# Optimization experiments

Hardware: AMD Instinct MI355X
Metric: run time of the kernel (lower is better)

The kernel has to match this reference:

```python
import jax, jax.numpy as jnp
import numpy as np

B, L_TOT, C = 64, 8192, 4
WIN = 16
H = 64
NL = 8
GROUPS = 8          # head groups
SA_GROUP = 4        # SortAttn group (hard-coded default)
GH = H * 2 // SA_GROUP   # 32
SEG = 4
CLS = 4
IN_SIZE = C * WIN   # 64 == H (all layers share input dim)


def _shuffle(x):
    # torch Shuffle: transpose(-1,-2).contiguous().view(original_shape)
    return jnp.swapaxes(x, -1, -2).reshape(x.shape)


def setup_inputs() -> dict:
    key = jax.random.key(0)
    ks = jax.random.split(key, 32)
    s = 0.1
    f32 = jnp.float32
    return {
        "x": jax.random.normal(ks[0], (B, L_TOT, C), f32),
        "h0_param": jnp.zeros((NL, 1, H), f32),
        "gru_w_ih": (jax.random.normal(ks[1], (NL, 3 * H, IN_SIZE), f32) * s),
        "gru_w_hh": (jax.random.normal(ks[2], (NL, 3 * H, H), f32) * s),
        "gru_b_ih": (jax.random.normal(ks[3], (NL, 3 * H), f32) * s),
        "gru_b_hh": (jax.random.normal(ks[4], (NL, 3 * H), f32) * s),
        "attn_w1": (jax.random.normal(ks[5], (NL, H, H), f32) * s),
        "attn_w2": (jax.random.normal(ks[6], (NL, GH, GH), f32) * s),
        "attn_w3": (jax.random.normal(ks[7], (NL, GH, GH), f32) * s),
        "attn_w4": (jax.random.normal(ks[8], (NL, H, 2 * H), f32) * s),
        "seg_w1": (jax.random.normal(ks[9], (SEG, H // GROUPS), f32) * s),
        "seg_b1": (jax.random.normal(ks[10], (SEG,), f32) * s),
        "seg_w2": (jax.random.normal(ks[11], (SEG, SEG), f32) * s),
        "seg_b2": (jax.random.normal(ks[12], (SEG,), f32) * s),
        "seg_w3": (jax.random.normal(ks[13], (SEG, SEG), f32) * s),
        "seg_b3": (jax.random.normal(ks[14], (SEG,), f32) * s),
        "seg_w4": (jax.random.normal(ks[15], (WIN, GROUPS), f32) * s),
        "seg_b4": (jax.random.normal(ks[16], (WIN,), f32) * s),
        "cls_w1": (jax.random.normal(ks[17], (CLS, H // GROUPS), f32) * s),
        "cls_b1": (jax.random.normal(ks[18], (CLS,), f32) * s),
        "cls_w2": (jax.random.normal(ks[19], (CLS, CLS), f32) * s),
        "cls_b2": (jax.random.normal(ks[20], (CLS,), f32) * s),
        "cls_w3": (jax.random.normal(ks[21], (CLS, CLS), f32) * s),
        "cls_b3": (jax.random.normal(ks[22], (CLS,), f32) * s),
        "cls_w4": (jax.random.normal(ks[23], (CLS, CLS * GROUPS), f32) * s),
        "cls_b4": (jax.random.normal(ks[24], (CLS,), f32) * s),
    }


def reference(x, h0_param, gru_w_ih, gru_w_hh, gru_b_ih, gru_b_hh,
              attn_w1, attn_w2, attn_w3, attn_w4,
              seg_w1, seg_b1, seg_w2, seg_b2, seg_w3, seg_b3, seg_w4, seg_b4,
              cls_w1, cls_b1, cls_w2, cls_b2, cls_w3, cls_b3, cls_w4, cls_b4):
    b, l, c = x.shape
    lw = l // WIN
    xs = x.reshape(b, lw, WIN * c)                     # (b, lw, IN_SIZE)
    h0 = jnp.broadcast_to(h0_param, (NL, b, H))        # hidden_0 * ones(1,b,1)

    def gru_cell(inp, h, w_ih, w_hh, b_ih, b_hh):
        gi = inp @ w_ih.T + b_ih                       # (b, 3H)
        gh = h @ w_hh.T + b_hh
        i_r, i_z, i_n = jnp.split(gi, 3, axis=1)
        h_r, h_z, h_n = jnp.split(gh, 3, axis=1)
        r = jax.nn.sigmoid(i_r + h_r)
        z = jax.nn.sigmoid(i_z + h_z)
        n = jnp.tanh(i_n + r * h_n)
        return (1.0 - z) * n + z * h

    def sort_attn(h, w1, w2, w3, w4):
        se = jnp.stack([h, jnp.sort(h, axis=1)], axis=1)   # (b, 2, H)
        a = se @ w1.T                                       # (b, 2, H)
        a = a.reshape(b, SA_GROUP, GH)                      # Flatten+Unflatten
        a = _shuffle(a) @ w2.T
        a = jax.nn.relu(_shuffle(a) @ w3.T)
        scores = jax.nn.sigmoid(a.reshape(b, SA_GROUP * GH) @ w4.T)  # (b, H)
        return h * scores

    def step(hidden, xt):
        inp = xt
        new = []
        for i in range(NL):
            hi = gru_cell(inp, hidden[i], gru_w_ih[i], gru_w_hh[i], gru_b_ih[i], gru_b_hh[i])
            hi = sort_attn(hi, attn_w1[i], attn_w2[i], attn_w3[i], attn_w4[i])
            new.append(hi)
            inp = hi
        return jnp.stack(new, axis=0), inp

    h_final, outs = jax.lax.scan(step, h0, jnp.swapaxes(xs, 0, 1))
    ys = jnp.swapaxes(outs, 0, 1)                      # (b, lw, H)

    # ---- seg head ----
    t = ys.reshape(b, lw, GROUPS, H // GROUPS)         # (b, lw, 8, 8)
    t = t @ seg_w1.T + seg_b1                          # (b, lw, 8, 4)
    t = _shuffle(t) @ seg_w2.T + seg_b2
    t = _shuffle(t) @ seg_w3.T + seg_b3
    t = t.reshape(b, lw, SEG, GROUPS)                  # Flatten(2)+Unflatten
    t = t @ seg_w4.T + seg_b4
    seg = jnp.swapaxes(t, -1, -2).reshape(b, lw * WIN, SEG)  # (b, l, 4)

    # ---- avg_pool1d(k=11, s=1) with 10 zero history frames ----
    pool_in = jnp.concatenate([jnp.zeros((b, 10, SEG), seg.dtype), seg], axis=1)
    cs = jnp.concatenate([jnp.zeros((b, 1, SEG), seg.dtype),
                          jnp.cumsum(pool_in, axis=1)], axis=1)
    pool_seg = (cs[:, 11:] - cs[:, :-11]) / 11.0       # (b, l, 4)

    # ---- cls head ----
    u = ys.reshape(b * lw, GROUPS, H // GROUPS)
    u = u @ cls_w1.T + cls_b1
    u = _shuffle(u) @ cls_w2.T + cls_b2
    u = jax.nn.relu(_shuffle(u) @ cls_w3.T + cls_b3)
    cls = u.reshape(b * lw, CLS * GROUPS) @ cls_w4.T + cls_b4
    cls = cls.reshape(b, lw, CLS).mean(axis=1)         # (b, 4)

    return (pool_seg, cls, ys, h_final, seg)
```

## Files before the change

kernel.cpp:

```cpp
#include <hip/hip_runtime.h>
#include <math.h>

#define LW  512

typedef unsigned short u16;
typedef float f32x4 __attribute__((ext_vector_type(4)));
typedef u16 u16x4 __attribute__((ext_vector_type(4)));
typedef u16 u16x8 __attribute__((ext_vector_type(8)));
typedef unsigned u32x2v __attribute__((ext_vector_type(2)));
typedef __bf16 bf16x8 __attribute__((ext_vector_type(8)));

__device__ __forceinline__ u16 f2bf(float f) {
    return __builtin_bit_cast(u16, (__bf16)f);
}
__device__ __forceinline__ float bf2f(u16 h) {
    unsigned u = ((unsigned)h) << 16;
    return __builtin_bit_cast(float, u);
}
__device__ __forceinline__ float sigm(float x) {
    return __builtin_amdgcn_rcpf(1.0f + __expf(-x));
}
__device__ __forceinline__ float tanhfast(float x) {
    return 1.0f - 2.0f * __builtin_amdgcn_rcpf(1.0f + __expf(2.0f * x));
}
__device__ __forceinline__ f32x4 mfma16(u16x8 a, u16x8 b, f32x4 c) {
    return __builtin_amdgcn_mfma_f32_16x16x32_bf16(
        __builtin_bit_cast(bf16x8, a), __builtin_bit_cast(bf16x8, b), c, 0, 0, 0);
}
__device__ __forceinline__ u16x8 ld8_8al(const u16* p) {
    u16x4 lo = *(const u16x4*)p;
    u16x4 hi = *(const u16x4*)(p + 4);
    return __builtin_shufflevector(lo, hi, 0, 1, 2, 3, 4, 5, 6, 7);
}
__device__ __forceinline__ unsigned ld_sys(const unsigned* p) {
    return __hip_atomic_load(p, __ATOMIC_RELAXED, __HIP_MEMORY_SCOPE_SYSTEM);
}
__device__ __forceinline__ void st_sys(unsigned* p, unsigned v) {
    __hip_atomic_store(p, v, __ATOMIC_RELAXED, __HIP_MEMORY_SCOPE_SYSTEM);
}
__device__ __forceinline__ void poll_ge(const unsigned* p, unsigned want) {
    while (ld_sys(p) < want) __builtin_amdgcn_s_sleep(2);
    asm volatile("" ::: "memory");
    __builtin_amdgcn_sched_barrier(0);
}
__device__ __forceinline__ void poll4(const unsigned* p, unsigned want) {
    for (;;) {
        unsigned m0 = ld_sys(p + 0), m1 = ld_sys(p + 1);
        unsigned m2 = ld_sys(p + 2), m3 = ld_sys(p + 3);
        unsigned a = m0 < m1 ? m0 : m1;
        unsigned b = m2 < m3 ? m2 : m3;
        if ((a < b ? a : b) >= want) break;
        __builtin_amdgcn_s_sleep(2);
    }
    asm volatile("" ::: "memory");
    __builtin_amdgcn_sched_barrier(0);
}
__device__ __forceinline__ void bar_lgkm() {
    asm volatile("s_waitcnt lgkmcnt(0)" ::: "memory");
    __builtin_amdgcn_s_barrier();
}

template<int CTRL> __device__ __forceinline__ float dppf(float v) {
    return __builtin_bit_cast(float,
        __builtin_amdgcn_mov_dpp(__builtin_bit_cast(int, v), CTRL, 0xF, 0xF, false));
}
template<int OFF> __device__ __forceinline__ float swzf(float v) {
    return __builtin_bit_cast(float,
        __builtin_amdgcn_ds_swizzle(__builtin_bit_cast(int, v), OFF));
}
template<int J> __device__ __forceinline__ float xch(float v) {
    if constexpr (J == 1)  return dppf<0xB1>(v);
    else if constexpr (J == 2)  return dppf<0x4E>(v);
    else if constexpr (J == 4)  return swzf<0x101F>(v);
    else if constexpr (J == 8)  return swzf<0x201F>(v);
    else if constexpr (J == 16) return swzf<0x401F>(v);
    else return __shfl_xor(v, 32);
}
#define STG(KK, J) { \
    float o0 = xch<J>(v0), o1 = xch<J>(v1); \
    bool keepmin = (((ln & KK) == 0) == ((ln & J) == 0)); \
    v0 = keepmin ? fminf(v0, o0) : fmaxf(v0, o0); \
    v1 = keepmin ? fminf(v1, o1) : fmaxf(v1, o1); }

__global__ __launch_bounds__(256) void init_flags(unsigned* f) {
    f[blockIdx.x * 256 + threadIdx.x] = 0u;
}

__global__ __launch_bounds__(256, 1) void rnn_kernel(
    const float* __restrict__ x, const float* __restrict__ h0,
    const float* __restrict__ w_ih, const float* __restrict__ w_hh,
    const float* __restrict__ bih, const float* __restrict__ bhh,
    const float* __restrict__ aw1, const float* __restrict__ aw2,
    const float* __restrict__ aw3, const float* __restrict__ aw4,
    float* __restrict__ ys, float* __restrict__ hfin,
    unsigned* __restrict__ flags, unsigned* __restrict__ ring32, int D)
{
    const int l   = blockIdx.x >> 3;
    const int g   = blockIdx.x & 7;
    const int bb0 = g * 8;
    const int tid = threadIdx.x;
    const int w   = tid >> 6;
    const int ln  = tid & 63;
    const int l15 = ln & 15;
    const int l4  = ln >> 4;
    const bool bp = (D < LW);

    unsigned* myflag = flags + (size_t)(l * 8 + g) * 32;
    unsigned* pflag  = flags + (size_t)((l - 1) * 8 + g) * 32;
    unsigned* myccnt = flags + 4096 + (size_t)(l * 8 + g) * 32;
    unsigned* nccnt  = flags + 4096 + (size_t)((l + 1) * 8 + g) * 32;

    __shared__ __align__(16) u16 Hin[2][16][72];
    __shared__ __align__(16) u16 hbf[16][72];
    __shared__ __align__(16) u16 se [16][72];
    __shared__ __align__(16) u16 a23[32][36];
    __shared__ __align__(16) u16 w4A[16][136];

    for (int i = tid; i < 16 * 72; i += 256) {
        int r = i / 72, c = i % 72;
        if (r >= 8) { Hin[0][r][c] = 0; Hin[1][r][c] = 0; hbf[r][c] = 0; }
    }
    for (int i = tid; i < 16 * 136; i += 256) {
        int r = i / 136;
        if (r >= 8) w4A[r][i % 136] = 0;
    }

    const int o = 16 * w + l15;
    auto ldw8 = [](const float* p) {
        float4 v0 = *(const float4*)p;
        float4 v1 = *(const float4*)(p + 4);
        u16x8 r;
        r[0] = f2bf(v0.x); r[1] = f2bf(v0.y); r[2] = f2bf(v0.z); r[3] = f2bf(v0.w);
        r[4] = f2bf(v1.x); r[5] = f2bf(v1.y); r[6] = f2bf(v1.z); r[7] = f2bf(v1.w);
        return r;
    };
    const float* ih = w_ih + l * 12288;
    const float* hh = w_hh + l * 12288;
    u16x8 Br[4], Bz[4], Bni[2], Bnh[2], B1f[2], B2f[2], B3f[2], B4f[4];
    Br[0] = ldw8(ih + o * 64 + l4 * 8);        Br[1] = ldw8(ih + o * 64 + 32 + l4 * 8);
    Br[2] = ldw8(hh + o * 64 + l4 * 8);        Br[3] = ldw8(hh + o * 64 + 32 + l4 * 8);
    Bz[0] = ldw8(ih + (64 + o) * 64 + l4 * 8); Bz[1] = ldw8(ih + (64 + o) * 64 + 32 + l4 * 8);
    Bz[2] = ldw8(hh + (64 + o) * 64 + l4 * 8); Bz[3] = ldw8(hh + (64 + o) * 64 + 32 + l4 * 8);
    Bni[0] = ldw8(ih + (128 + o) * 64 + l4 * 8); Bni[1] = ldw8(ih + (128 + o) * 64 + 32 + l4 * 8);
    Bnh[0] = ldw8(hh + (128 + o) * 64 + l4 * 8); Bnh[1] = ldw8(hh + (128 + o) * 64 + 32 + l4 * 8);
    B1f[0] = ldw8(aw1 + l * 4096 + o * 64 + l4 * 8);
    B1f[1] = ldw8(aw1 + l * 4096 + o * 64 + 32 + l4 * 8);
    B2f[0] = ldw8(aw2 + l * 1024 + l15 * 32 + l4 * 8);
    B2f[1] = ldw8(aw2 + l * 1024 + (16 + l15) * 32 + l4 * 8);
    B3f[0] = ldw8(aw3 + l * 1024 + l15 * 32 + l4 * 8);
    B3f[1] = ldw8(aw3 + l * 1024 + (16 + l15) * 32 + l4 * 8);
    #pragma unroll
    for (int kk = 0; kk < 4; ++kk)
        B4f[kk] = ldw8(aw4 + l * 8192 + o * 128 + kk * 32 + l4 * 8);

    const float brs  = bih[l * 192 + o]       + bhh[l * 192 + o];
    const float bzs  = bih[l * 192 + 64 + o]  + bhh[l * 192 + 64 + o];
    const float bnis = bih[l * 192 + 128 + o];
    const float bnhs = bhh[l * 192 + 128 + o];

    float hreg[4];
    {
        float hv = h0[l * 64 + o];
        #pragma unroll
        for (int j = 0; j < 4; ++j) hreg[j] = hv;
        if (l4 < 2) {
            u16 hb = f2bf(hv);
            #pragma unroll
            for (int j = 0; j < 4; ++j) hbf[l4 * 4 + j][o] = hb;
        }
    }

    float4 stf = {0.f, 0.f, 0.f, 0.f};
    unsigned st0 = 0, st1 = 0;
    if (w >= 2) {
        const int rr = (tid - 128) >> 4, c4 = ((tid - 128) & 15) * 4;
        if (l == 0) {
            float4 a = *(const float4*)(x + (size_t)(bb0 + rr) * 32768 + c4);
            u16x4 hv;
            hv[0] = f2bf(a.x); hv[1] = f2bf(a.y); hv[2] = f2bf(a.z); hv[3] = f2bf(a.w);
            *(u16x4*)&Hin[0][rr][c4] = hv;
            stf = *(const float4*)(x + (size_t)(bb0 + rr) * 32768 + 64 + c4);
        } else {
            poll4(pflag, 1u);
            const unsigned* sp0 = ring32 + ((size_t)((l - 1) * 8 + g) * D + 0) * 256 + rr * 32 + (c4 >> 1);
            unsigned a0 = ld_sys(sp0), a1 = ld_sys(sp0 + 1);
            u32x2v dv = {a0, a1};
            *(u16x4*)&Hin[0][rr][c4] = __builtin_bit_cast(u16x4, dv);
            poll4(pflag, 2u);
            const unsigned* sp1 = ring32 + ((size_t)((l - 1) * 8 + g) * D + 1) * 256 + rr * 32 + (c4 >> 1);
            st0 = ld_sys(sp1); st1 = ld_sys(sp1 + 1);
        }
    }
    __syncthreads();

    u16x8 pAg0 = *(const u16x8*)&Hin[0][l15][l4 * 8];
    u16x8 pAg1 = *(const u16x8*)&Hin[0][l15][32 + l4 * 8];

    for (int t = 0; t < LW; ++t) {
        float hg[4];
        {
            u16x8 Ah0 = *(const u16x8*)&hbf[l15][l4 * 8];
            u16x8 Ah1 = *(const u16x8*)&hbf[l15][32 + l4 * 8];
            f32x4 z4 = {0.f, 0.f, 0.f, 0.f};
            f32x4 aR = z4, aZ = z4, aNI = z4, aNH = z4;
            aR = mfma16(pAg0, Br[0], aR);  aR = mfma16(pAg1, Br[1], aR);
            aR = mfma16(Ah0, Br[2], aR);   aR = mfma16(Ah1, Br[3], aR);
            aZ = mfma16(pAg0, Bz[0], aZ);  aZ = mfma16(pAg1, Bz[1], aZ);
            aZ = mfma16(Ah0, Bz[2], aZ);   aZ = mfma16(Ah1, Bz[3], aZ);
            aNI = mfma16(pAg0, Bni[0], aNI); aNI = mfma16(pAg1, Bni[1], aNI);
            aNH = mfma16(Ah0, Bnh[0], aNH);  aNH = mfma16(Ah1, Bnh[1], aNH);
            #pragma unroll
            for (int j = 0; j < 4; ++j) {
                float r  = sigm(aR[j] + brs);
                float zz = sigm(aZ[j] + bzs);
                float nn = tanhfast(aNI[j] + bnis + r * (aNH[j] + bnhs));
                hg[j] = (1.0f - zz) * nn + zz * hreg[j];
            }
            if (l4 < 2) {
                #pragma unroll
                for (int j = 0; j < 4; ++j) se[l4 * 4 + j][o] = f2bf(hg[j]);
            }
        }
        bar_lgkm();

        {
            float v0 = bf2f(se[2 * w][ln]);
            float v1 = bf2f(se[2 * w + 1][ln]);
            STG(2, 1)
            STG(4, 2)  STG(4, 1)
            STG(8, 4)  STG(8, 2)  STG(8, 1)
            STG(16, 8) STG(16, 4) STG(16, 2) STG(16, 1)
            STG(32, 16) STG(32, 8) STG(32, 4) STG(32, 2) STG(32, 1)
            STG(64, 32) STG(64, 16) STG(64, 8) STG(64, 4) STG(64, 2) STG(64, 1)
            se[8 + 2 * w][ln] = f2bf(v0);
            se[9 + 2 * w][ln] = f2bf(v1);
        }
        bar_lgkm();

        if (l < 7) {
            asm volatile("s_waitcnt vmcnt(0)" ::: "memory");
            if (ln == 0) st_sys(myflag + w, (unsigned)t);
        }
        {
            u16x8 As0 = *(const u16x8*)&se[l15][l4 * 8];
            u16x8 As1 = *(const u16x8*)&se[l15][32 + l4 * 8];
            f32x4 c = {0.f, 0.f, 0.f, 0.f};
            c = mfma16(As0, B1f[0], c);
            c = mfma16(As1, B1f[1], c);
            #pragma unroll
            for (int j = 0; j < 4; ++j) {
                int m = l4 * 4 + j;
                int p = m >> 3, b = m & 7;
                int f = p * 64 + o;
                int q = (f & 31) * 4 + (f >> 5);
                a23[b * 4 + (q >> 5)][q & 31] = f2bf(c[j]);
            }
        }
        bar_lgkm();

        if (w < 2) {
            const int Rb0 = 16 * w;
            u16x8 a2a = ld8_8al(&a23[Rb0 + l15][l4 * 8]);
            f32x4 z4 = {0.f, 0.f, 0.f, 0.f};
            f32x4 c2[2];
            c2[0] = mfma16(a2a, B2f[0], z4);
            c2[1] = mfma16(a2a, B2f[1], z4);
            #pragma unroll
            for (int nt = 0; nt < 2; ++nt)
                #pragma unroll
                for (int j = 0; j < 4; ++j) {
                    int m = Rb0 + l4 * 4 + j;
                    int b = m >> 2, i2 = m & 3;
                    int n = 16 * nt + l15;
                    int f2 = i2 * 32 + n;
                    int q2 = (f2 & 31) * 4 + (f2 >> 5);
                    a23[b * 4 + (q2 >> 5)][q2 & 31] = f2bf(c2[nt][j]);
                }
            asm volatile("s_waitcnt lgkmcnt(0)" ::: "memory");
            __builtin_amdgcn_sched_barrier(0);
            u16x8 a3a = ld8_8al(&a23[Rb0 + l15][l4 * 8]);
            f32x4 c3[2];
            c3[0] = mfma16(a3a, B3f[0], z4);
            c3[1] = mfma16(a3a, B3f[1], z4);
            #pragma unroll
            for (int nt = 0; nt < 2; ++nt)
                #pragma unroll
                for (int j = 0; j < 4; ++j) {
                    int m = Rb0 + l4 * 4 + j;
                    int b = m >> 2, i3 = m & 3;
                    int n = 16 * nt + l15;
                    w4A[b][i3 * 32 + n] = f2bf(fmaxf(c3[nt][j], 0.0f));
                }
        } else {
            const int rr = (tid - 128) >> 4, c4 = ((tid - 128) & 15) * 4;
            if (t + 1 < LW) {
                u16x4 hv;
                if (l == 0) {
                    hv[0] = f2bf(stf.x); hv[1] = f2bf(stf.y);
                    hv[2] = f2bf(stf.z); hv[3] = f2bf(stf.w);
                } else {
                    u32x2v dv = {st0, st1};
                    hv = __builtin_bit_cast(u16x4, dv);
                }
                *(u16x4*)&Hin[(t + 1) & 1][rr][c4] = hv;
            }
            if (t + 2 < LW) {
                if (l == 0) {
                    stf = *(const float4*)(x + (size_t)(bb0 + rr) * 32768 + (t + 2) * 64 + c4);
                } else {
                    poll4(pflag, (unsigned)(t + 3));
                    const unsigned* sp = ring32
                        + ((size_t)((l - 1) * 8 + g) * D + ((t + 2) & (D - 1))) * 256
                        + rr * 32 + (c4 >> 1);
                    st0 = ld_sys(sp); st1 = ld_sys(sp + 1);
                }
            }
        }
        bar_lgkm();
        if (bp && l > 0 && tid == 0)
            st_sys(myccnt, (unsigned)(t + 2));

        {
            u16x8 A40 = *(const u16x8*)&w4A[l15][l4 * 8];
            u16x8 A41 = *(const u16x8*)&w4A[l15][32 + l4 * 8];
            u16x8 A42 = *(const u16x8*)&w4A[l15][64 + l4 * 8];
            u16x8 A43 = *(const u16x8*)&w4A[l15][96 + l4 * 8];
            pAg0 = *(const u16x8*)&Hin[(t + 1) & 1][l15][l4 * 8];
            pAg1 = *(const u16x8*)&Hin[(t + 1) & 1][l15][32 + l4 * 8];
            f32x4 cs = {0.f, 0.f, 0.f, 0.f};
            cs = mfma16(A40, B4f[0], cs);
            cs = mfma16(A41, B4f[1], cs);
            cs = mfma16(A42, B4f[2], cs);
            cs = mfma16(A43, B4f[3], cs);

            if (bp && l < 7 && t >= D) {
                poll_ge(nccnt, (unsigned)(t - D + 1));
            }
            unsigned* slotp = ring32 + ((size_t)(l * 8 + g) * D + (t & (D - 1))) * 256;
            float hn[4]; u16 hb[4];
            #pragma unroll
            for (int j = 0; j < 4; ++j) {
                hn[j] = hg[j] * sigm(cs[j]);
                hreg[j] = hn[j];
                hb[j] = f2bf(hn[j]);
            }
            if (l4 < 2) {
                #pragma unroll
                for (int j = 0; j < 4; ++j) {
                    int row = l4 * 4 + j;
                    hbf[row][o] = hb[j];
                    if (l == 7) ys[(((size_t)(bb0 + row) << 9) + t) * 64 + o] = hn[j];
                    if (t == 511) hfin[((l << 6) + bb0 + row) * 64 + o] = hn[j];
                }
            }
            if (l < 7) {
                #pragma unroll
                for (int j = 0; j < 4; ++j) {
                    unsigned ob = (unsigned)__shfl_xor((int)(unsigned)hb[j], 1) & 0xffffu;
                    if (l4 < 2 && !(l15 & 1)) {
                        unsigned word = (unsigned)hb[j] | (ob << 16);
                        st_sys(&slotp[(l4 * 4 + j) * 32 + (o >> 1)], word);
                    }
                }
            }
        }
        bar_lgkm();
    }

    if (l < 7) {
        asm volatile("s_waitcnt vmcnt(0)" ::: "memory");
        if (ln == 0) st_sys(myflag + w, 512u);
    }
}

__global__ __launch_bounds__(256) void heads_kernel(
    const float* __restrict__ ys,
    const float* __restrict__ sw1, const float* __restrict__ sb1,
    const float* __restrict__ sw2, const float* __restrict__ sb2,
    const float* __restrict__ sw3, const float* __restrict__ sb3,
    const float* __restrict__ sw4, const float* __restrict__ sb4,
    const float* __restrict__ cw1, const float* __restrict__ cb1,
    const float* __restrict__ cw2, const float* __restrict__ cb2,
    const float* __restrict__ cw3, const float* __restrict__ cb3,
    const float* __restrict__ cw4, const float* __restrict__ cb4,
    float* __restrict__ seg_out, float* __restrict__ cls_tmp)
{
    const int idx = blockIdx.x * 256 + threadIdx.x;
    if (idx >= 64 * LW) return;
    const int b = idx >> 9, t = idx & 511;

    float y[64];
    const float4* yp = (const float4*)(ys + (size_t)idx * 64);
    #pragma unroll
    for (int i = 0; i < 16; ++i) {
        float4 v = yp[i];
        y[4 * i + 0] = v.x; y[4 * i + 1] = v.y; y[4 * i + 2] = v.z; y[4 * i + 3] = v.w;
    }

    float t1[8][4], t2[8][4], t3[8][4];

    #pragma unroll
    for (int g = 0; g < 8; ++g)
        #pragma unroll
        for (int s = 0; s < 4; ++s) {
            float acc = sb1[s];
            #pragma unroll
            for (int k = 0; k < 8; ++k) acc = fmaf(y[g * 8 + k], sw1[s * 8 + k], acc);
            t1[g][s] = acc;
        }
    #pragma unroll
    for (int i = 0; i < 8; ++i) {
        float sh[4];
        #pragma unroll
        for (int j = 0; j < 4; ++j) { int m = i * 4 + j; sh[j] = t1[m & 7][m >> 3]; }
        #pragma unroll
        for (int s = 0; s < 4; ++s) {
            float acc = sb2[s];
            #pragma unroll
            for (int j = 0; j < 4; ++j) acc = fmaf(sh[j], sw2[s * 4 + j], acc);
            t2[i][s] = acc;
        }
    }
    #pragma unroll
    for (int i = 0; i < 8; ++i) {
        float sh[4];
        #pragma unroll
        for (int j = 0; j < 4; ++j) { int m = i * 4 + j; sh[j] = t2[m & 7][m >> 3]; }
        #pragma unroll
        for (int s = 0; s < 4; ++s) {
            float acc = sb3[s];
            #pragma unroll
            for (int j = 0; j < 4; ++j) acc = fmaf(sh[j], sw3[s * 4 + j], acc);
            t3[i][s] = acc;
        }
    }
    #pragma unroll
    for (int w = 0; w < 16; ++w) {
        float o4[4];
        #pragma unroll
        for (int s = 0; s < 4; ++s) {
            float acc = sb4[w];
            #pragma unroll
            for (int j = 0; j < 8; ++j) {
                int f = s * 8 + j;
                acc = fmaf(t3[f >> 2][f & 3], sw4[w * 8 + j], acc);
            }
            o4[s] = acc;
        }
        float4 vv = {o4[0], o4[1], o4[2], o4[3]};
        ((float4*)seg_out)[b * 8192 + t * 16 + w] = vv;
    }

    #pragma unroll
    for (int g = 0; g < 8; ++g)
        #pragma unroll
        for (int s = 0; s < 4; ++s) {
            float acc = cb1[s];
            #pragma unroll
            for (int k = 0; k < 8; ++k) acc = fmaf(y[g * 8 + k], cw1[s * 8 + k], acc);
            t1[g][s] = acc;
        }
    #pragma unroll
    for (int i = 0; i < 8; ++i) {
        float sh[4];
        #pragma unroll
        for (int j = 0; j < 4; ++j) { int m = i * 4 + j; sh[j] = t1[m & 7][m >> 3]; }
        #pragma unroll
        for (int s = 0; s < 4; ++s) {
            float acc = cb2[s];
            #pragma unroll
            for (int j = 0; j < 4; ++j) acc = fmaf(sh[j], cw2[s * 4 + j], acc);
            t2[i][s] = acc;
        }
    }
    #pragma unroll
    for (int i = 0; i < 8; ++i) {
        float sh[4];
        #pragma unroll
        for (int j = 0; j < 4; ++j) { int m = i * 4 + j; sh[j] = t2[m & 7][m >> 3]; }
        #pragma unroll
        for (int s = 0; s < 4; ++s) {
            float acc = cb3[s];
            #pragma unroll
            for (int j = 0; j < 4; ++j) acc = fmaf(sh[j], cw3[s * 4 + j], acc);
            t3[i][s] = fmaxf(acc, 0.f);
        }
    }
    float cc[4];
    #pragma unroll
    for (int c = 0; c < 4; ++c) {
        float acc = cb4[c];
        #pragma unroll
        for (int k = 0; k < 32; ++k)
            acc = fmaf(t3[k >> 2][k & 3], cw4[c * 32 + k], acc);
        cc[c] = acc;
    }
    float4 cv = {cc[0], cc[1], cc[2], cc[3]};
    ((float4*)cls_tmp)[idx] = cv;
}

__global__ __launch_bounds__(256) void cls_reduce_kernel(
    const float* __restrict__ cls_tmp, float* __restrict__ cls_out)
{
    const int tid = threadIdx.x;
    const int b = tid >> 2, q = tid & 3;
    float ax = 0.f, ay = 0.f, az = 0.f, aw = 0.f;
    for (int t = q; t < 512; t += 4) {
        float4 v = ((const float4*)cls_tmp)[b * 512 + t];
        ax += v.x; ay += v.y; az += v.z; aw += v.w;
    }
    ax += __shfl_xor(ax, 1); ay += __shfl_xor(ay, 1);
    az += __shfl_xor(az, 1); aw += __shfl_xor(aw, 1);
    ax += __shfl_xor(ax, 2); ay += __shfl_xor(ay, 2);
    az += __shfl_xor(az, 2); aw += __shfl_xor(aw, 2);
    if (q == 0) {
        float4 rv = {ax / 512.f, ay / 512.f, az / 512.f, aw / 512.f};
        ((float4*)cls_out)[b] = rv;
    }
}

__global__ __launch_bounds__(256) void pool_kernel(
    const float* __restrict__ seg, float* __restrict__ pool_out)
{
    const int idx = blockIdx.x * 256 + threadIdx.x;
    if (idx >= 64 * 8192) return;
    const int b = idx >> 13, ll = idx & 8191;
    float ax = 0.f, ay = 0.f, az = 0.f, aw = 0.f;
    int j0 = ll - 10; if (j0 < 0) j0 = 0;
    for (int j = j0; j <= ll; ++j) {
        float4 v = ((const float4*)seg)[b * 8192 + j];
        ax += v.x; ay += v.y; az += v.z; aw += v.w;
    }
    const float inv = 1.0f / 11.0f;
    float4 ov = {ax * inv, ay * inv, az * inv, aw * inv};
    ((float4*)pool_out)[idx] = ov;
}

extern "C" void kernel_launch(void* const* d_in, const int* in_sizes, int n_in,
                              void* d_out, int out_size, void* d_ws, size_t ws_size,
                              hipStream_t stream)
{
    const float* x    = (const float*)d_in[0];
    const float* h0   = (const float*)d_in[1];
    const float* w_ih = (const float*)d_in[2];
    const float* w_hh = (const float*)d_in[3];
    const float* bihp = (const float*)d_in[4];
    const float* bhhp = (const float*)d_in[5];
    const float* aw1  = (const float*)d_in[6];
    const float* aw2  = (const float*)d_in[7];
    const float* aw3  = (const float*)d_in[8];
    const float* aw4  = (const float*)d_in[9];
    const float* sw1  = (const float*)d_in[10];
    const float* sb1  = (const float*)d_in[11];
    const float* sw2  = (const float*)d_in[12];
    const float* sb2  = (const float*)d_in[13];
    const float* sw3  = (const float*)d_in[14];
    const float* sb3  = (const float*)d_in[15];
    const float* sw4  = (const float*)d_in[16];
    const float* sb4  = (const float*)d_in[17];
    const float* cw1  = (const float*)d_in[18];
    const float* cb1  = (const float*)d_in[19];
    const float* cw2  = (const float*)d_in[20];
    const float* cb2  = (const float*)d_in[21];
    const float* cw3  = (const float*)d_in[22];
    const float* cb3  = (const float*)d_in[23];
    const float* cw4  = (const float*)d_in[24];
    const float* cb4  = (const float*)d_in[25];

    float* out      = (float*)d_out;
    float* pool_out = out;
    float* cls_out  = out + 2097152;
    float* ys_out   = out + 2097408;
    float* hfin     = out + 4194560;
    float* seg_out  = out + 4227328;
    float* cls_tmp  = pool_out;

    unsigned* flags  = (unsigned*)d_ws;
    unsigned* ring32 = (unsigned*)((char*)d_ws + 32768);

    size_t slots = (ws_size > 32768) ? (ws_size - 32768) / (56ull * 256 * 4) : 8;
    int D = 512;
    if (slots < 512) {
        D = 8;
        while ((size_t)(D * 2) <= slots && D < 512) D <<= 1;
    }

    init_flags<<<32, 256, 0, stream>>>(flags);
    rnn_kernel<<<64, 256, 0, stream>>>(x, h0, w_ih, w_hh, bihp, bhhp,
                                       aw1, aw2, aw3, aw4, ys_out, hfin,
                                       flags, ring32, D);
    heads_kernel<<<128, 256, 0, stream>>>(ys_out, sw1, sb1, sw2, sb2, sw3, sb3, sw4, sb4,
                                          cw1, cb1, cw2, cb2, cw3, cb3, cw4, cb4,
                                          seg_out, cls_tmp);
    cls_reduce_kernel<<<1, 256, 0, stream>>>(cls_tmp, cls_out);
    pool_kernel<<<2048, 256, 0, stream>>>(seg_out, pool_out);
}
```

Baseline: 1.350 ms.

## Precompose attention linear maps W1·shuffle·W2·shuffle·W3 into one matrix per layer

Adds a prep kernel that multiplies the attention weights w1, w2 and w3, with the shuffle permutations folded in, into a single 128x128 bf16 matrix per layer, which is stored in workspace. The per-step attention in the recurrent kernel becomes one K=128 MFMA pass over the concatenated [h, sorted h] row instead of three dependent MFMA stages, each with an LDS scatter and a barrier. This is meant to shorten the serial per-timestep critical path. The cost is more MFMAs per step, one extra small launch, and a change in bf16 rounding because the intermediate products are no longer rounded.

```diff
diff --git a/kernel.cpp b/kernel.cpp
--- a/kernel.cpp
+++ b/kernel.cpp
@@ -26,11 +26,6 @@
 __device__ __forceinline__ f32x4 mfma16(u16x8 a, u16x8 b, f32x4 c) {
     return __builtin_amdgcn_mfma_f32_16x16x32_bf16(
         __builtin_bit_cast(bf16x8, a), __builtin_bit_cast(bf16x8, b), c, 0, 0, 0);
-}
-__device__ __forceinline__ u16x8 ld8_8al(const u16* p) {
-    u16x4 lo = *(const u16x4*)p;
-    u16x4 hi = *(const u16x4*)(p + 4);
-    return __builtin_shufflevector(lo, hi, 0, 1, 2, 3, 4, 5, 6, 7);
 }
 __device__ __forceinline__ unsigned ld_sys(const unsigned* p) {
     return __hip_atomic_load(p, __ATOMIC_RELAXED, __HIP_MEMORY_SCOPE_SYSTEM);
@@ -76,22 +71,68 @@
     else if constexpr (J == 16) return swzf<0x401F>(v);
     else return __shfl_xor(v, 32);
 }
-#define STG(KK, J) { \
-    float o0 = xch<J>(v0), o1 = xch<J>(v1); \
-    bool keepmin = (((ln & KK) == 0) == ((ln & J) == 0)); \
-    v0 = keepmin ? fminf(v0, o0) : fmaxf(v0, o0); \
-    v1 = keepmin ? fminf(v1, o1) : fmaxf(v1, o1); }
+#define STG4(KK, J) { \
+    float o0 = xch<J>(v0), o1 = xch<J>(v1), o2 = xch<J>(v2), o3 = xch<J>(v3); \
+    bool k = (((ln & KK) == 0) == ((ln & J) == 0)); \
+    v0 = k ? fminf(v0, o0) : fmaxf(v0, o0); \
+    v1 = k ? fminf(v1, o1) : fmaxf(v1, o1); \
+    v2 = k ? fminf(v2, o2) : fmaxf(v2, o2); \
+    v3 = k ? fminf(v3, o3) : fmaxf(v3, o3); }
 
 __global__ __launch_bounds__(256) void init_flags(unsigned* f) {
     f[blockIdx.x * 256 + threadIdx.x] = 0u;
+}
+
+__global__ __launch_bounds__(128) void prep_A(
+    const float* __restrict__ aw1, const float* __restrict__ aw2,
+    const float* __restrict__ aw3, u16* __restrict__ Abf)
+{
+    const int l   = blockIdx.x;
+    const int tid = threadIdx.x;
+    __shared__ float T1[128][65];
+    __shared__ float T2[128][65];
+    for (int ch = 0; ch < 2; ++ch) {
+        for (int i = tid; i < 128 * 64; i += 128) {
+            int f = i >> 6, j = i & 63;
+            int s = ch * 64 + j;
+            T1[f][j] = ((f >> 6) == (s >> 6))
+                       ? aw1[l * 4096 + (f & 63) * 64 + (s & 63)] : 0.f;
+        }
+        __syncthreads();
+        for (int i = tid; i < 128 * 64; i += 128) {
+            int gg = i >> 6, j = i & 63;
+            int n = gg & 31, r = gg >> 5;
+            float acc = 0.f;
+            #pragma unroll 8
+            for (int k = 0; k < 32; ++k) {
+                int g = r * 32 + k;
+                int src = (g & 3) * 32 + (g >> 2);
+                acc += aw2[l * 1024 + n * 32 + k] * T1[src][j];
+            }
+            T2[gg][j] = acc;
+        }
+        __syncthreads();
+        for (int i = tid; i < 128 * 64; i += 128) {
+            int ff = i >> 6, j = i & 63;
+            int n = ff & 31, r = ff >> 5;
+            float acc = 0.f;
+            #pragma unroll 8
+            for (int k = 0; k < 32; ++k) {
+                int g = r * 32 + k;
+                int src = (g & 3) * 32 + (g >> 2);
+                acc += aw3[l * 1024 + n * 32 + k] * T2[src][j];
+            }
+            Abf[((size_t)l * 128 + ff) * 128 + ch * 64 + j] = f2bf(acc);
+        }
+        __syncthreads();
+    }
 }
 
 __global__ __launch_bounds__(256, 1) void rnn_kernel(
     const float* __restrict__ x, const float* __restrict__ h0,
     const float* __restrict__ w_ih, const float* __restrict__ w_hh,
     const float* __restrict__ bih, const float* __restrict__ bhh,
-    const float* __restrict__ aw1, const float* __restrict__ aw2,
-    const float* __restrict__ aw3, const float* __restrict__ aw4,
+    const u16* __restrict__ Abf, const float* __restrict__ aw4,
     float* __restrict__ ys, float* __restrict__ hfin,
     unsigned* __restrict__ flags, unsigned* __restrict__ ring32, int D)
 {
@@ -112,8 +153,7 @@
 
     __shared__ __align__(16) u16 Hin[2][16][72];
     __shared__ __align__(16) u16 hbf[16][72];
-    __shared__ __align__(16) u16 se [16][72];
-    __shared__ __align__(16) u16 a23[32][36];
+    __shared__ __align__(16) u16 seF[16][136];
     __shared__ __align__(16) u16 w4A[16][136];
 
     for (int i = tid; i < 16 * 72; i += 256) {
@@ -122,7 +162,7 @@
     }
     for (int i = tid; i < 16 * 136; i += 256) {
         int r = i / 136;
-        if (r >= 8) w4A[r][i % 136] = 0;
+        if (r >= 8) { w4A[r][i % 136] = 0; seF[r][i % 136] = 0; }
     }
 
     const int o = 16 * w + l15;
@@ -136,22 +176,22 @@
     };
     const float* ih = w_ih + l * 12288;
     const float* hh = w_hh + l * 12288;
-    u16x8 Br[4], Bz[4], Bni[2], Bnh[2], B1f[2], B2f[2], B3f[2], B4f[4];
+    u16x8 Br[4], Bz[4], Bni[2], Bnh[2], B4f[4], BA[2][4];
     Br[0] = ldw8(ih + o * 64 + l4 * 8);        Br[1] = ldw8(ih + o * 64 + 32 + l4 * 8);
     Br[2] = ldw8(hh + o * 64 + l4 * 8);        Br[3] = ldw8(hh + o * 64 + 32 + l4 * 8);
     Bz[0] = ldw8(ih + (64 + o) * 64 + l4 * 8); Bz[1] = ldw8(ih + (64 + o) * 64 + 32 + l4 * 8);
     Bz[2] = ldw8(hh + (64 + o) * 64 + l4 * 8); Bz[3] = ldw8(hh + (64 + o) * 64 + 32 + l4 * 8);
     Bni[0] = ldw8(ih + (128 + o) * 64 + l4 * 8); Bni[1] = ldw8(ih + (128 + o) * 64 + 32 + l4 * 8);
     Bnh[0] = ldw8(hh + (128 + o) * 64 + l4 * 8); Bnh[1] = ldw8(hh + (128 + o) * 64 + 32 + l4 * 8);
-    B1f[0] = ldw8(aw1 + l * 4096 + o * 64 + l4 * 8);
-    B1f[1] = ldw8(aw1 + l * 4096 + o * 64 + 32 + l4 * 8);
-    B2f[0] = ldw8(aw2 + l * 1024 + l15 * 32 + l4 * 8);
-    B2f[1] = ldw8(aw2 + l * 1024 + (16 + l15) * 32 + l4 * 8);
-    B3f[0] = ldw8(aw3 + l * 1024 + l15 * 32 + l4 * 8);
-    B3f[1] = ldw8(aw3 + l * 1024 + (16 + l15) * 32 + l4 * 8);
     #pragma unroll
     for (int kk = 0; kk < 4; ++kk)
         B4f[kk] = ldw8(aw4 + l * 8192 + o * 128 + kk * 32 + l4 * 8);
+    #pragma unroll
+    for (int nt = 0; nt < 2; ++nt)
+        #pragma unroll
+        for (int kk = 0; kk < 4; ++kk)
+            BA[nt][kk] = *(const u16x8*)&Abf[((size_t)l * 128 + (16 * (2 * w + nt) + l15)) * 128
+                                             + kk * 32 + l4 * 8];
 
     const float brs  = bih[l * 192 + o]       + bhh[l * 192 + o];
     const float bzs  = bih[l * 192 + 64 + o]  + bhh[l * 192 + 64 + o];
@@ -218,79 +258,27 @@
             }
             if (l4 < 2) {
                 #pragma unroll
-                for (int j = 0; j < 4; ++j) se[l4 * 4 + j][o] = f2bf(hg[j]);
+                for (int j = 0; j < 4; ++j) seF[l4 * 4 + j][o] = f2bf(hg[j]);
             }
         }
         bar_lgkm();
 
-        {
-            float v0 = bf2f(se[2 * w][ln]);
-            float v1 = bf2f(se[2 * w + 1][ln]);
-            STG(2, 1)
-            STG(4, 2)  STG(4, 1)
-            STG(8, 4)  STG(8, 2)  STG(8, 1)
-            STG(16, 8) STG(16, 4) STG(16, 2) STG(16, 1)
-            STG(32, 16) STG(32, 8) STG(32, 4) STG(32, 2) STG(32, 1)
-            STG(64, 32) STG(64, 16) STG(64, 8) STG(64, 4) STG(64, 2) STG(64, 1)
-            se[8 + 2 * w][ln] = f2bf(v0);
-            se[9 + 2 * w][ln] = f2bf(v1);
-        }
-        bar_lgkm();
-
-        if (l < 7) {
-            asm volatile("s_waitcnt vmcnt(0)" ::: "memory");
-            if (ln == 0) st_sys(myflag + w, (unsigned)t);
-        }
-        {
-            u16x8 As0 = *(const u16x8*)&se[l15][l4 * 8];
-            u16x8 As1 = *(const u16x8*)&se[l15][32 + l4 * 8];
-            f32x4 c = {0.f, 0.f, 0.f, 0.f};
-            c = mfma16(As0, B1f[0], c);
-            c = mfma16(As1, B1f[1], c);
-            #pragma unroll
-            for (int j = 0; j < 4; ++j) {
-                int m = l4 * 4 + j;
-                int p = m >> 3, b = m & 7;
-                int f = p * 64 + o;
-                int q = (f & 31) * 4 + (f >> 5);
-                a23[b * 4 + (q >> 5)][q & 31] = f2bf(c[j]);
-            }
-        }
-        bar_lgkm();
-
         if (w < 2) {
-            const int Rb0 = 16 * w;
-            u16x8 a2a = ld8_8al(&a23[Rb0 + l15][l4 * 8]);
-            f32x4 z4 = {0.f, 0.f, 0.f, 0.f};
-            f32x4 c2[2];
-            c2[0] = mfma16(a2a, B2f[0], z4);
-            c2[1] = mfma16(a2a, B2f[1], z4);
-            #pragma unroll
-            for (int nt = 0; nt < 2; ++nt)
-                #pragma unroll
-                for (int j = 0; j < 4; ++j) {
-                    int m = Rb0 + l4 * 4 + j;
-                    int b = m >> 2, i2 = m & 3;
-                    int n = 16 * nt + l15;
-                    int f2 = i2 * 32 + n;
-                    int q2 = (f2 & 31) * 4 + (f2 >> 5);
-                    a23[b * 4 + (q2 >> 5)][q2 & 31] = f2bf(c2[nt][j]);
-                }
-            asm volatile("s_waitcnt lgkmcnt(0)" ::: "memory");
-            __builtin_amdgcn_sched_barrier(0);
-            u16x8 a3a = ld8_8al(&a23[Rb0 + l15][l4 * 8]);
-            f32x4 c3[2];
-            c3[0] = mfma16(a3a, B3f[0], z4);
-            c3[1] = mfma16(a3a, B3f[1], z4);
-            #pragma unroll
-            for (int nt = 0; nt < 2; ++nt)
-                #pragma unroll
-                for (int j = 0; j < 4; ++j) {
-                    int m = Rb0 + l4 * 4 + j;
-                    int b = m >> 2, i3 = m & 3;
-                    int n = 16 * nt + l15;
-                    w4A[b][i3 * 32 + n] = f2bf(fmaxf(c3[nt][j], 0.0f));
-                }
+            const int r0 = 4 * w;
+            float v0 = bf2f(seF[r0 + 0][ln]);
+            float v1 = bf2f(seF[r0 + 1][ln]);
+            float v2 = bf2f(seF[r0 + 2][ln]);
+            float v3 = bf2f(seF[r0 + 3][ln]);
+            STG4(2, 1)
+            STG4(4, 2)  STG4(4, 1)
+            STG4(8, 4)  STG4(8, 2)  STG4(8, 1)
+            STG4(16, 8) STG4(16, 4) STG4(16, 2) STG4(16, 1)
+            STG4(32, 16) STG4(32, 8) STG4(32, 4) STG4(32, 2) STG4(32, 1)
+            STG4(64, 32) STG4(64, 16) STG4(64, 8) STG4(64, 4) STG4(64, 2) STG4(64, 1)
+            seF[r0 + 0][64 + ln] = f2bf(v0);
+            seF[r0 + 1][64 + ln] = f2bf(v1);
+            seF[r0 + 2][64 + ln] = f2bf(v2);
+            seF[r0 + 3][64 + ln] = f2bf(v3);
         } else {
             const int rr = (tid - 128) >> 4, c4 = ((tid - 128) & 15) * 4;
             if (t + 1 < LW) {
@@ -319,6 +307,32 @@
         bar_lgkm();
         if (bp && l > 0 && tid == 0)
             st_sys(myccnt, (unsigned)(t + 2));
+
+        if (l < 7) {
+            asm volatile("s_waitcnt vmcnt(0)" ::: "memory");
+            if (ln == 0) st_sys(myflag + w, (unsigned)t);
+        }
+        {
+            u16x8 As0 = *(const u16x8*)&seF[l15][l4 * 8];
+            u16x8 As1 = *(const u16x8*)&seF[l15][32 + l4 * 8];
+            u16x8 As2 = *(const u16x8*)&seF[l15][64 + l4 * 8];
+            u16x8 As3 = *(const u16x8*)&seF[l15][96 + l4 * 8];
+            f32x4 z4 = {0.f, 0.f, 0.f, 0.f};
+            f32x4 c0 = z4, c1 = z4;
+            c0 = mfma16(As0, BA[0][0], c0); c0 = mfma16(As1, BA[0][1], c0);
+            c0 = mfma16(As2, BA[0][2], c0); c0 = mfma16(As3, BA[0][3], c0);
+            c1 = mfma16(As0, BA[1][0], c1); c1 = mfma16(As1, BA[1][1], c1);
+            c1 = mfma16(As2, BA[1][2], c1); c1 = mfma16(As3, BA[1][3], c1);
+            if (l4 < 2) {
+                #pragma unroll
+                for (int j = 0; j < 4; ++j) {
+                    int m = l4 * 4 + j;
+                    w4A[m][16 * (2 * w + 0) + l15] = f2bf(fmaxf(c0[j], 0.0f));
+                    w4A[m][16 * (2 * w + 1) + l15] = f2bf(fmaxf(c1[j], 0.0f));
+                }
+            }
+        }
+        bar_lgkm();
 
         {
             u16x8 A40 = *(const u16x8*)&w4A[l15][l4 * 8];
@@ -576,9 +590,11 @@
     float* cls_tmp  = pool_out;
 
     unsigned* flags  = (unsigned*)d_ws;
-    unsigned* ring32 = (unsigned*)((char*)d_ws + 32768);
-
-    size_t slots = (ws_size > 32768) ? (ws_size - 32768) / (56ull * 256 * 4) : 8;
+    u16*      Abf    = (u16*)((char*)d_ws + 32768);
+    unsigned* ring32 = (unsigned*)((char*)d_ws + 32768 + 262144);
+
+    size_t hdr = 32768 + 262144;
+    size_t slots = (ws_size > hdr) ? (ws_size - hdr) / (56ull * 256 * 4) : 8;
     int D = 512;
     if (slots < 512) {
         D = 8;
@@ -586,8 +602,9 @@
     }
 
     init_flags<<<32, 256, 0, stream>>>(flags);
+    prep_A<<<8, 128, 0, stream>>>(aw1, aw2, aw3, Abf);
     rnn_kernel<<<64, 256, 0, stream>>>(x, h0, w_ih, w_hh, bihp, bhhp,
-                                       aw1, aw2, aw3, aw4, ys_out, hfin,
+                                       Abf, aw4, ys_out, hfin,
                                        flags, ring32, D);
     heads_kernel<<<128, 256, 0, stream>>>(ys_out, sw1, sb1, sw2, sb2, sw3, sb3, sw4, sb4,
                                           cw1, cb1, cw2, cb2, cw3, cb3, cw4, cb4,
```

Result: slower. 1.599 ms (+18.4%).
